# Kernel optimization log

Measured on AMD Instinct MI355X. Metric: run time of the kernel, lower is better.

## Reference

```python
import jax, jax.numpy as jnp
import numpy as np

B, S, D, H, HD = 4, 2048, 1024, 16, 64  # batch, seq, d_model, heads, head_dim


def setup_inputs() -> dict:
    key = jax.random.key(0)
    ks = jax.random.split(key, 9)
    scale = 0.02
    x = jax.random.normal(ks[0], (B, S, D), jnp.float32)
    Wq = jax.random.normal(ks[1], (D, H, HD), jnp.float32) * scale
    Wk = jax.random.normal(ks[2], (D, H, HD), jnp.float32) * scale
    Wv = jax.random.normal(ks[3], (D, H, HD), jnp.float32) * scale
    bq = jax.random.normal(ks[4], (H, HD), jnp.float32) * scale
    bk = jax.random.normal(ks[5], (H, HD), jnp.float32) * scale
    bv = jax.random.normal(ks[6], (H, HD), jnp.float32) * scale
    Wo = jax.random.normal(ks[7], (H, HD, D), jnp.float32) * scale
    bo = jax.random.normal(ks[8], (D,), jnp.float32) * scale
    return {"x": x, "Wq": Wq, "bq": bq, "Wk": Wk, "bk": bk,
            "Wv": Wv, "bv": bv, "Wo": Wo, "bo": bo}


def reference(x, Wq, bq, Wk, bk, Wv, bv, Wo, bo):
    # QKV projections -> (B, S, H, HD)
    q = jnp.einsum("bsd,dhe->bshe", x, Wq) + bq
    k = jnp.einsum("bsd,dhe->bshe", x, Wk) + bk
    v = jnp.einsum("bsd,dhe->bshe", x, Wv) + bv
    # scaled dot-product attention (deterministic, no mask/bias)
    q = q / jnp.sqrt(jnp.asarray(HD, q.dtype))
    scores = jnp.einsum("bqhd,bkhd->bhqk", q, k)  # (B, H, S, S)
    attn = jax.nn.softmax(scores, axis=-1)
    ctx = jnp.einsum("bhqk,bkhd->bqhd", attn, v)  # (B, S, H, HD)
    # output projection -> (B, S, D)
    return jnp.einsum("bqhd,hdo->bqo", ctx, Wo) + bo
```

## Files before the change

### kernel.cpp

```cpp
#include <hip/hip_runtime.h>


typedef unsigned short u16;
typedef __attribute__((ext_vector_type(4))) float f32x4;
typedef __attribute__((ext_vector_type(8))) short s16x8;
typedef __attribute__((ext_vector_type(4))) unsigned short u16x4;
typedef __attribute__((ext_vector_type(2))) unsigned int u32x2;
typedef __attribute__((ext_vector_type(4))) unsigned int u32x4;

#define DEV __device__ __forceinline__

#if __has_builtin(__builtin_amdgcn_exp2f)
#define EXP2(x) __builtin_amdgcn_exp2f(x)
#else
#define EXP2(x) exp2f(x)
#endif

DEV u16 f2b(float f) {
  unsigned u = __float_as_uint(f);
  u += 0x7fffu + ((u >> 16) & 1u);
  return (u16)(u >> 16);
}

DEV unsigned pack2(float a, float b) {
#if __has_builtin(__builtin_amdgcn_cvt_pk_bf16_f32)
  typedef __attribute__((ext_vector_type(2))) __bf16 bf16x2;
  bf16x2 r = __builtin_amdgcn_cvt_pk_bf16_f32(a, b);
  return __builtin_bit_cast(unsigned, r);
#else
  return (unsigned)f2b(a) | ((unsigned)f2b(b) << 16);
#endif
}

DEV void async16(const void* g, void* l) {
  __builtin_amdgcn_global_load_lds(
      (const __attribute__((address_space(1))) unsigned int*)g,
      (__attribute__((address_space(3))) unsigned int*)l, 16, 0, 0);
}

__global__ void k_cast(const float* __restrict__ x, u16* __restrict__ xb) {
  int i = (blockIdx.x * 256 + threadIdx.x) * 4;
  float4 v = *(const float4*)(x + i);
  u16x4 o;
  o.x = f2b(v.x); o.y = f2b(v.y); o.z = f2b(v.z); o.w = f2b(v.w);
  *(u16x4*)(xb + i) = o;
}

__global__ void k_packw_all(const float* __restrict__ Wq, const float* __restrict__ Wk,
                            const float* __restrict__ Wv, const float* __restrict__ Wo,
                            u16* __restrict__ wt, u16* __restrict__ wot, float qscale) {
  const float* src; u16* dst; float scale = 1.0f;
  switch (blockIdx.z) {
    case 0: src = Wq; dst = wt; scale = qscale; break;
    case 1: src = Wk; dst = wt + 1024 * 1024; break;
    case 2: src = Wv; dst = wt + 2 * 1024 * 1024; break;
    default: src = Wo; dst = wot; break;
  }
  __shared__ float tile[32][33];
  int t = threadIdx.x;
  int k0 = blockIdx.x * 32, n0 = blockIdx.y * 32;
  int c = t & 31, r0 = t >> 5;
#pragma unroll
  for (int p = 0; p < 4; ++p) {
    int r = p * 8 + r0;
    tile[r][c] = src[(size_t)(k0 + r) * 1024 + n0 + c] * scale;
  }
  __syncthreads();
#pragma unroll
  for (int p = 0; p < 4; ++p) {
    int r = p * 8 + r0;
    dst[(size_t)(n0 + r) * 1024 + k0 + c] = f2b(tile[c][r]);
  }
}

__global__ void k_packbias(const float* __restrict__ bq, const float* __restrict__ bk,
                           const float* __restrict__ bv, float* __restrict__ out,
                           float qscale) {
  int t = blockIdx.x * 256 + threadIdx.x;
  float v = (t < 1024) ? bq[t] * qscale : (t < 2048 ? bk[t - 1024] : bv[t - 2048]);
  out[t] = v;
}

template <int MODE>
__global__ __launch_bounds__(256, 2) void k_gemm_bt(
    const u16* __restrict__ A, const u16* __restrict__ Bt,
    const float* __restrict__ bias, void* __restrict__ Cout, u16* __restrict__ VT,
    int K, int ldC, int nbase) {
  __shared__ u16 SH[16384];
  u16* As = SH;
  u16* Bs = SH + 8192;
  const int t = threadIdx.x;
  const int w = t >> 6, l = t & 63;
  const int lane15 = l & 15, quad = l >> 4;
  const int m0 = blockIdx.x * 128, n0 = nbase + blockIdx.y * 128;
  const int wm = (w >> 1) * 64, wn = (w & 1) * 64;

  const int srow = t >> 3, cp = t & 7;
  const u16* aSrc[4]; const u16* bSrc[4]; int ldsOff[4];
#pragma unroll
  for (int i = 0; i < 4; ++i) {
    int row = i * 32 + srow;
    int gc = cp ^ (row & 7);
    aSrc[i] = A + (size_t)(m0 + row) * K + gc * 8;
    bSrc[i] = Bt + (size_t)(n0 + row) * K + gc * 8;
    ldsOff[i] = (i * 32 + w * 8) * 64;
  }

  f32x4 acc[4][4] = {};

  for (int kk = 0; kk < K; kk += 64) {
#pragma unroll
    for (int i = 0; i < 4; ++i) async16(aSrc[i] + kk, As + ldsOff[i]);
#pragma unroll
    for (int i = 0; i < 4; ++i) async16(bSrc[i] + kk, Bs + ldsOff[i]);
    __builtin_amdgcn_s_waitcnt(0);
    __syncthreads();

#pragma unroll
    for (int ks = 0; ks < 2; ++ks) {
      s16x8 af[4], bf[4];
#pragma unroll
      for (int mi = 0; mi < 4; ++mi) {
        int r = wm + mi * 16 + lane15;
        int c = ks * 4 + quad;
        af[mi] = *(const s16x8*)(As + r * 64 + (c ^ (r & 7)) * 8);
      }
#pragma unroll
      for (int ni = 0; ni < 4; ++ni) {
        int r = wn + ni * 16 + lane15;
        int c = ks * 4 + quad;
        bf[ni] = *(const s16x8*)(Bs + r * 64 + (c ^ (r & 7)) * 8);
      }
#pragma unroll
      for (int mi = 0; mi < 4; ++mi)
#pragma unroll
        for (int ni = 0; ni < 4; ++ni)
          acc[mi][ni] = (MODE == 0)
              ? __builtin_amdgcn_mfma_f32_16x16x32_bf16(bf[ni], af[mi], acc[mi][ni], 0, 0, 0)
              : __builtin_amdgcn_mfma_f32_16x16x32_bf16(af[mi], bf[ni], acc[mi][ni], 0, 0, 0);
    }
    __syncthreads();
  }

  if (MODE == 0) {
    u16* W = SH + w * 4096;
#pragma unroll
    for (int ni = 0; ni < 4; ++ni) {
      int gnb = n0 + wn + ni * 16 + quad * 4;
      float4 bb = *(const float4*)(bias + gnb);
#pragma unroll
      for (int mi = 0; mi < 4; ++mi) {
        int mloc = mi * 16 + lane15;
        int nloc = ni * 16 + quad * 4;
        int blk = (nloc >> 3) ^ (mloc & 7);
        u32x2 o;
        o.x = pack2(acc[mi][ni][0] + bb.x, acc[mi][ni][1] + bb.y);
        o.y = pack2(acc[mi][ni][2] + bb.z, acc[mi][ni][3] + bb.w);
        *(u32x2*)(W + mloc * 64 + blk * 8 + (quad & 1) * 4) = o;
      }
    }
    const int l8 = l & 7, lr = l >> 3;
#pragma unroll
    for (int it = 0; it < 8; ++it) {
      int mloc = it * 8 + lr;
      int lb = l8 ^ (mloc & 7);
      s16x8 v = *(const s16x8*)(W + mloc * 64 + l8 * 8);
      int gm = m0 + wm + mloc;
      *(s16x8*)((u16*)Cout + (size_t)gm * ldC + n0 + wn + lb * 8) = v;
    }
  } else if (MODE == 1) {
#pragma unroll
    for (int ni = 0; ni < 4; ++ni) {
      int gn = n0 + wn + ni * 16 + lane15;
      float bb = bias[gn];
#pragma unroll
      for (int mi = 0; mi < 4; ++mi) {
        int gmBase = m0 + wm + mi * 16 + quad * 4;
#pragma unroll
        for (int r = 0; r < 4; ++r)
          ((float*)Cout)[(size_t)(gmBase + r) * ldC + gn] = acc[mi][ni][r] + bb;
      }
    }
  } else {
    u16* W = SH + w * 4096;
#pragma unroll
    for (int ni = 0; ni < 4; ++ni) {
      int gn = n0 + wn + ni * 16 + lane15;
      float bb = bias[gn];
#pragma unroll
      for (int mi = 0; mi < 4; ++mi) {
        int nloc = ni * 16 + lane15;
        int mloc = mi * 16 + quad * 4;
        int blk = (mloc >> 3) ^ (nloc & 7);
        u32x2 o;
        o.x = pack2(acc[mi][ni][0] + bb, acc[mi][ni][1] + bb);
        o.y = pack2(acc[mi][ni][2] + bb, acc[mi][ni][3] + bb);
        *(u32x2*)(W + nloc * 64 + blk * 8 + (quad & 1) * 4) = o;
      }
    }
    const int l8 = l & 7, lr = l >> 3;
#pragma unroll
    for (int it = 0; it < 8; ++it) {
      int nloc = it * 8 + lr;
      int lb = l8 ^ (nloc & 7);
      s16x8 v = *(const s16x8*)(W + nloc * 64 + l8 * 8);
      int gv = (n0 - 2048) + wn + nloc;
      int hh = gv >> 6, hd = gv & 63;
      int gm = m0 + wm + lb * 8;
      int bb2 = gm >> 11, s = gm & 2047;
      *(s16x8*)(VT + (((size_t)(bb2 * 16 + hh) * 64 + hd) * 2048 + s)) = v;
    }
  }
}

__global__ __launch_bounds__(512, 4) void k_flash(
    const u16* __restrict__ qkv, const u16* __restrict__ vt, u16* __restrict__ ctx) {
  __shared__ u16 S[2][8192];
  const int t = threadIdx.x;
  const int w = t >> 6, l = t & 63;
  const int lane15 = l & 15, quad = l >> 4;
  const int bh = blockIdx.x, qt = blockIdx.y;
  const int b = bh >> 4, h = bh & 15;

  int qrow[2];
  s16x8 qf[2][2];
#pragma unroll
  for (int T = 0; T < 2; ++T) {
    qrow[T] = b * 2048 + qt * 256 + w * 32 + T * 16 + lane15;
    const u16* qp = qkv + (size_t)qrow[T] * 2048 + h * 64 + quad * 8;
    qf[T][0] = *(const s16x8*)(qp);
    qf[T][1] = *(const s16x8*)(qp + 32);
  }

  const int srow = t >> 3, cp = t & 7;
  const int xks = (srow & 3) | (((srow >> 3) & 1) << 2);
  const u16* kSrc = qkv + (size_t)(b * 2048 + srow) * 2048 + 1024 + h * 64 + (cp ^ xks) * 8;
  const u16* vSrc = vt + (size_t)bh * (64 * 2048) + (size_t)srow * 2048 + (cp ^ (srow & 7)) * 8;
  const int kOff = w * 512;
  const int vOff = 4096 + w * 512;

  const int kr = (lane15 >> 2) * 8 + (lane15 & 3);
  f32x4 O[2][4] = {};
  float lsum[2] = {0.0f, 0.0f};
  const f32x4 ZERO4 = {};

  async16(kSrc, &S[0][kOff]);
  async16(vSrc, &S[0][vOff]);

  for (int jt = 0; jt < 32; ++jt) {
    __builtin_amdgcn_s_waitcnt(0);
    __syncthreads();
    const u16* Sb = S[jt & 1];
    if (jt < 31) {
      const size_t kAdv = (size_t)(jt + 1) * 64 * 2048;
      const int vAdv = (jt + 1) * 64;
      u16* D = S[(jt & 1) ^ 1];
      async16(kSrc + kAdv, D + kOff);
      async16(vSrc + vAdv, D + vOff);
    }

    f32x4 st[2][4];
    __builtin_amdgcn_s_setprio(1);
#pragma unroll
    for (int tt = 0; tt < 4; ++tt) {
      int rr = kr + (tt & 1) * 4 + (tt >> 1) * 32;
      int xk = (rr & 3) | (((rr >> 3) & 1) << 2);
      s16x8 kf = *(const s16x8*)(Sb + rr * 64 + ((0 * 4 + quad) ^ xk) * 8);
#pragma unroll
      for (int T = 0; T < 2; ++T)
        st[T][tt] = __builtin_amdgcn_mfma_f32_16x16x32_bf16(kf, qf[T][0], ZERO4, 0, 0, 0);
    }
#pragma unroll
    for (int tt = 0; tt < 4; ++tt) {
      int rr = kr + (tt & 1) * 4 + (tt >> 1) * 32;
      int xk = (rr & 3) | (((rr >> 3) & 1) << 2);
      s16x8 kf = *(const s16x8*)(Sb + rr * 64 + ((1 * 4 + quad) ^ xk) * 8);
#pragma unroll
      for (int T = 0; T < 2; ++T)
        st[T][tt] = __builtin_amdgcn_mfma_f32_16x16x32_bf16(kf, qf[T][1], st[T][tt], 0, 0, 0);
    }
    __builtin_amdgcn_s_setprio(0);

#pragma unroll
    for (int ks = 0; ks < 2; ++ks) {
      s16x8 pf[2];
#pragma unroll
      for (int T = 0; T < 2; ++T) {
        float p0 = EXP2(st[T][2 * ks][0]), p1 = EXP2(st[T][2 * ks][1]);
        float p2 = EXP2(st[T][2 * ks][2]), p3 = EXP2(st[T][2 * ks][3]);
        float p4 = EXP2(st[T][2 * ks + 1][0]), p5 = EXP2(st[T][2 * ks + 1][1]);
        float p6 = EXP2(st[T][2 * ks + 1][2]), p7 = EXP2(st[T][2 * ks + 1][3]);
        lsum[T] += ((p0 + p1) + (p2 + p3)) + ((p4 + p5) + (p6 + p7));
        u32x4 pu = {pack2(p0, p1), pack2(p2, p3), pack2(p4, p5), pack2(p6, p7)};
        pf[T] = __builtin_bit_cast(s16x8, pu);
      }
      const u16* Vh = Sb + 4096;
      int c7 = ks * 4 + quad;
      __builtin_amdgcn_s_setprio(1);
#pragma unroll
      for (int co = 0; co < 4; ++co) {
        int rr = co * 16 + lane15;
        s16x8 vf = *(const s16x8*)(Vh + rr * 64 + ((c7 ^ (rr & 7))) * 8);
#pragma unroll
        for (int T = 0; T < 2; ++T)
          O[T][co] = __builtin_amdgcn_mfma_f32_16x16x32_bf16(vf, pf[T], O[T][co], 0, 0, 0);
      }
      __builtin_amdgcn_s_setprio(0);
    }
  }

#pragma unroll
  for (int T = 0; T < 2; ++T) {
    lsum[T] += __shfl_xor(lsum[T], 16);
    lsum[T] += __shfl_xor(lsum[T], 32);
  }

#pragma unroll
  for (int T = 0; T < 2; ++T) {
    float inv = 1.0f / lsum[T];
#pragma unroll
    for (int co = 0; co < 4; ++co) {
      u32x2 o;
      o.x = pack2(O[T][co][0] * inv, O[T][co][1] * inv);
      o.y = pack2(O[T][co][2] * inv, O[T][co][3] * inv);
      *(u32x2*)(ctx + (size_t)qrow[T] * 1024 + h * 64 + co * 16 + quad * 4) = o;
    }
  }
}

static constexpr size_t OFF_XB  = 0;
static constexpr size_t OFF_WT  = OFF_XB + (16u << 20);
static constexpr size_t OFF_WOT = OFF_WT + (6u << 20);
static constexpr size_t OFF_B3  = OFF_WOT + (2u << 20);
static constexpr size_t OFF_QKV = OFF_B3 + (1u << 20);
static constexpr size_t OFF_VT  = OFF_QKV + (32u << 20);
static constexpr size_t OFF_CTX = OFF_VT + (16u << 20);

extern "C" void kernel_launch(void* const* d_in, const int* in_sizes, int n_in,
                              void* d_out, int out_size, void* d_ws, size_t ws_size,
                              hipStream_t stream) {
  const float* x  = (const float*)d_in[0];
  const float* Wq = (const float*)d_in[1];
  const float* bq = (const float*)d_in[2];
  const float* Wk = (const float*)d_in[3];
  const float* bk = (const float*)d_in[4];
  const float* Wv = (const float*)d_in[5];
  const float* bv = (const float*)d_in[6];
  const float* Wo = (const float*)d_in[7];
  const float* bo = (const float*)d_in[8];
  char* ws = (char*)d_ws;
  u16* xb    = (u16*)(ws + OFF_XB);
  u16* wt    = (u16*)(ws + OFF_WT);
  u16* wot   = (u16*)(ws + OFF_WOT);
  float* b3  = (float*)(ws + OFF_B3);
  u16* qkv   = (u16*)(ws + OFF_QKV);
  u16* vtb   = (u16*)(ws + OFF_VT);
  u16* ctx   = (u16*)(ws + OFF_CTX);
  float* out = (float*)d_out;

  const float QSCALE = 0.125f * 1.44269504f;

  k_cast<<<8192, 256, 0, stream>>>(x, xb);
  k_packw_all<<<dim3(32, 32, 4), 256, 0, stream>>>(Wq, Wk, Wv, Wo, wt, wot, QSCALE);
  k_packbias<<<12, 256, 0, stream>>>(bq, bk, bv, b3, QSCALE);
  k_gemm_bt<0><<<dim3(64, 16), 256, 0, stream>>>(xb, wt, b3, qkv, nullptr, 1024, 2048, 0);
  k_gemm_bt<2><<<dim3(64, 8), 256, 0, stream>>>(xb, wt, b3, nullptr, vtb, 1024, 2048, 2048);
  k_flash<<<dim3(64, 8), 512, 0, stream>>>(qkv, vtb, ctx);
  k_gemm_bt<1><<<dim3(64, 8), 256, 0, stream>>>(ctx, wot, bo, out, nullptr, 1024, 1024, 0);
}
```

Measured before the change: 265.8 us.

## Load K/V fragments directly from global memory in flash kernel, drop LDS staging

Removes the double-buffered shared-memory staging of K and V tiles and the per-iteration barrier. Each wave now loads its MFMA operand fragments straight from global memory, relying on L1/L2 caching across waves. The block is halved to 256 threads over 128 query rows, with the grid doubled to match. This trades barrier and LDS overhead for redundant global loads by every wave and the latency of exposed global reads.

```diff
diff --git a/kernel.cpp b/kernel.cpp
--- a/kernel.cpp
+++ b/kernel.cpp
@@ -213,9 +213,8 @@
   }
 }
 
-__global__ __launch_bounds__(512, 4) void k_flash(
+__global__ __launch_bounds__(256, 4) void k_flash(
     const u16* __restrict__ qkv, const u16* __restrict__ vt, u16* __restrict__ ctx) {
-  __shared__ u16 S[2][8192];
   const int t = threadIdx.x;
   const int w = t >> 6, l = t & 63;
   const int lane15 = l & 15, quad = l >> 4;
@@ -226,63 +225,58 @@
   s16x8 qf[2][2];
 #pragma unroll
   for (int T = 0; T < 2; ++T) {
-    qrow[T] = b * 2048 + qt * 256 + w * 32 + T * 16 + lane15;
+    qrow[T] = b * 2048 + qt * 128 + w * 32 + T * 16 + lane15;
     const u16* qp = qkv + (size_t)qrow[T] * 2048 + h * 64 + quad * 8;
     qf[T][0] = *(const s16x8*)(qp);
     qf[T][1] = *(const s16x8*)(qp + 32);
   }
 
-  const int srow = t >> 3, cp = t & 7;
-  const int xks = (srow & 3) | (((srow >> 3) & 1) << 2);
-  const u16* kSrc = qkv + (size_t)(b * 2048 + srow) * 2048 + 1024 + h * 64 + (cp ^ xks) * 8;
-  const u16* vSrc = vt + (size_t)bh * (64 * 2048) + (size_t)srow * 2048 + (cp ^ (srow & 7)) * 8;
-  const int kOff = w * 512;
-  const int vOff = 4096 + w * 512;
-
   const int kr = (lane15 >> 2) * 8 + (lane15 & 3);
+  const u16* kBase = qkv + (size_t)b * 2048 * 2048 + 1024 + h * 64 + quad * 8;
+  const u16* vBase = vt + (size_t)bh * (64 * 2048) + quad * 8;
+  int kOffE[4], vOffE[4];
+#pragma unroll
+  for (int tt = 0; tt < 4; ++tt) kOffE[tt] = (kr + (tt & 1) * 4 + (tt >> 1) * 32) * 2048;
+#pragma unroll
+  for (int co = 0; co < 4; ++co) vOffE[co] = (co * 16 + lane15) * 2048;
+
   f32x4 O[2][4] = {};
   float lsum[2] = {0.0f, 0.0f};
   const f32x4 ZERO4 = {};
 
-  async16(kSrc, &S[0][kOff]);
-  async16(vSrc, &S[0][vOff]);
-
   for (int jt = 0; jt < 32; ++jt) {
-    __builtin_amdgcn_s_waitcnt(0);
-    __syncthreads();
-    const u16* Sb = S[jt & 1];
-    if (jt < 31) {
-      const size_t kAdv = (size_t)(jt + 1) * 64 * 2048;
-      const int vAdv = (jt + 1) * 64;
-      u16* D = S[(jt & 1) ^ 1];
-      async16(kSrc + kAdv, D + kOff);
-      async16(vSrc + vAdv, D + vOff);
+    const u16* kT = kBase + (size_t)jt * 64 * 2048;
+    const u16* vT = vBase + jt * 64;
+
+    s16x8 kf0[4], kf1[4];
+#pragma unroll
+    for (int tt = 0; tt < 4; ++tt) {
+      const u16* p = kT + kOffE[tt];
+      kf0[tt] = *(const s16x8*)(p);
+      kf1[tt] = *(const s16x8*)(p + 32);
     }
 
     f32x4 st[2][4];
     __builtin_amdgcn_s_setprio(1);
 #pragma unroll
-    for (int tt = 0; tt < 4; ++tt) {
-      int rr = kr + (tt & 1) * 4 + (tt >> 1) * 32;
-      int xk = (rr & 3) | (((rr >> 3) & 1) << 2);
-      s16x8 kf = *(const s16x8*)(Sb + rr * 64 + ((0 * 4 + quad) ^ xk) * 8);
+    for (int tt = 0; tt < 4; ++tt)
 #pragma unroll
       for (int T = 0; T < 2; ++T)
-        st[T][tt] = __builtin_amdgcn_mfma_f32_16x16x32_bf16(kf, qf[T][0], ZERO4, 0, 0, 0);
-    }
-#pragma unroll
-    for (int tt = 0; tt < 4; ++tt) {
-      int rr = kr + (tt & 1) * 4 + (tt >> 1) * 32;
-      int xk = (rr & 3) | (((rr >> 3) & 1) << 2);
-      s16x8 kf = *(const s16x8*)(Sb + rr * 64 + ((1 * 4 + quad) ^ xk) * 8);
+        st[T][tt] = __builtin_amdgcn_mfma_f32_16x16x32_bf16(kf0[tt], qf[T][0], ZERO4, 0, 0, 0);
+#pragma unroll
+    for (int tt = 0; tt < 4; ++tt)
 #pragma unroll
       for (int T = 0; T < 2; ++T)
-        st[T][tt] = __builtin_amdgcn_mfma_f32_16x16x32_bf16(kf, qf[T][1], st[T][tt], 0, 0, 0);
-    }
+        st[T][tt] = __builtin_amdgcn_mfma_f32_16x16x32_bf16(kf1[tt], qf[T][1], st[T][tt], 0, 0, 0);
     __builtin_amdgcn_s_setprio(0);
 
 #pragma unroll
     for (int ks = 0; ks < 2; ++ks) {
+      s16x8 vf[4];
+#pragma unroll
+      for (int co = 0; co < 4; ++co)
+        vf[co] = *(const s16x8*)(vT + vOffE[co] + ks * 32);
+
       s16x8 pf[2];
 #pragma unroll
       for (int T = 0; T < 2; ++T) {
@@ -294,17 +288,13 @@
         u32x4 pu = {pack2(p0, p1), pack2(p2, p3), pack2(p4, p5), pack2(p6, p7)};
         pf[T] = __builtin_bit_cast(s16x8, pu);
       }
-      const u16* Vh = Sb + 4096;
-      int c7 = ks * 4 + quad;
+
       __builtin_amdgcn_s_setprio(1);
 #pragma unroll
-      for (int co = 0; co < 4; ++co) {
-        int rr = co * 16 + lane15;
-        s16x8 vf = *(const s16x8*)(Vh + rr * 64 + ((c7 ^ (rr & 7))) * 8);
+      for (int co = 0; co < 4; ++co)
 #pragma unroll
         for (int T = 0; T < 2; ++T)
-          O[T][co] = __builtin_amdgcn_mfma_f32_16x16x32_bf16(vf, pf[T], O[T][co], 0, 0, 0);
-      }
+          O[T][co] = __builtin_amdgcn_mfma_f32_16x16x32_bf16(vf[co], pf[T], O[T][co], 0, 0, 0);
       __builtin_amdgcn_s_setprio(0);
     }
   }
@@ -365,6 +355,6 @@
   k_packbias<<<12, 256, 0, stream>>>(bq, bk, bv, b3, QSCALE);
   k_gemm_bt<0><<<dim3(64, 16), 256, 0, stream>>>(xb, wt, b3, qkv, nullptr, 1024, 2048, 0);
   k_gemm_bt<2><<<dim3(64, 8), 256, 0, stream>>>(xb, wt, b3, nullptr, vtb, 1024, 2048, 2048);
-  k_flash<<<dim3(64, 8), 512, 0, stream>>>(qkv, vtb, ctx);
+  k_flash<<<dim3(64, 16), 256, 0, stream>>>(qkv, vtb, ctx);
   k_gemm_bt<1><<<dim3(64, 8), 256, 0, stream>>>(ctx, wot, bo, out, nullptr, 1024, 1024, 0);
 }
```

Result: slower. 504.9 us (+90.0%).

## Fuse QKV projections into one double-buffered 128x256 GEMM kernel

Applied to the files above, without the earlier changes.

Replaces the two QKV projection GEMM launches (Q/K to a row-major buffer, V to a transposed buffer) with a single kernel. It uses 512 threads, 128x256 tiles and double-buffered LDS, so the next K-tile loads asynchronously while the current one runs MFMA. MFMA sections run at raised wave priority and use split barriers. This removes one launch and the exposed load latency of the old single-buffered loop, at the cost of 96KB LDS and one block per CU.

```diff
diff --git a/kernel.cpp b/kernel.cpp
--- a/kernel.cpp
+++ b/kernel.cpp
@@ -79,6 +79,144 @@
   int t = blockIdx.x * 256 + threadIdx.x;
   float v = (t < 1024) ? bq[t] * qscale : (t < 2048 ? bk[t - 1024] : bv[t - 2048]);
   out[t] = v;
+}
+
+#define QKV_STAGE(DST, kn)                                                \
+  { const int ko = (kn) * 64;                                             \
+    async16(aB + ko,          (DST) + 0 * 4096 + w * 512);                \
+    async16(aB + 65536 + ko,  (DST) + 4096 + w * 512);                    \
+    async16(bB + ko,          (DST) + 8192 + w * 512);                    \
+    async16(bB + 65536 + ko,  (DST) + 12288 + w * 512);                   \
+    async16(bB + 131072 + ko, (DST) + 16384 + w * 512);                   \
+    async16(bB + 196608 + ko, (DST) + 20480 + w * 512); }
+
+#define QKV_LOADFRAG(SRC, ks)                                             \
+  { _Pragma("unroll") for (int mi = 0; mi < 4; ++mi) {                    \
+      int r = wmE + mi * 16 + lane15;                                     \
+      int c = (ks) * 4 + quad;                                            \
+      af[mi] = *(const s16x8*)((SRC) + r * 64 + (c ^ (r & 7)) * 8);       \
+    }                                                                     \
+    _Pragma("unroll") for (int ni = 0; ni < 4; ++ni) {                    \
+      int rn = wnE + ni * 16 + lane15;                                    \
+      int c = (ks) * 4 + quad;                                            \
+      bf[ni] = *(const s16x8*)((SRC) + 8192 + rn * 64 + (c ^ (rn & 7)) * 8); \
+    } }
+
+#define QKV_MFMA()                                                        \
+  { __builtin_amdgcn_s_setprio(1);                                        \
+    if (swapped) {                                                        \
+      _Pragma("unroll") for (int mi = 0; mi < 4; ++mi)                    \
+        _Pragma("unroll") for (int ni = 0; ni < 4; ++ni)                  \
+          acc[mi][ni] = __builtin_amdgcn_mfma_f32_16x16x32_bf16(          \
+              bf[ni], af[mi], acc[mi][ni], 0, 0, 0);                      \
+    } else {                                                              \
+      _Pragma("unroll") for (int mi = 0; mi < 4; ++mi)                    \
+        _Pragma("unroll") for (int ni = 0; ni < 4; ++ni)                  \
+          acc[mi][ni] = __builtin_amdgcn_mfma_f32_16x16x32_bf16(          \
+              af[mi], bf[ni], acc[mi][ni], 0, 0, 0);                      \
+    }                                                                     \
+    __builtin_amdgcn_s_setprio(0); }
+
+#define QKV_TILE(SRC, DST, kt, DO_STAGE)                                  \
+  { if (DO_STAGE) QKV_STAGE(DST, (kt) + 1);                               \
+    s16x8 af[4], bf[4];                                                   \
+    QKV_LOADFRAG(SRC, 0);                                                 \
+    __builtin_amdgcn_s_barrier();                                         \
+    QKV_MFMA();                                                           \
+    __builtin_amdgcn_s_barrier();                                         \
+    QKV_LOADFRAG(SRC, 1);                                                 \
+    __builtin_amdgcn_s_barrier();                                         \
+    QKV_MFMA();                                                           \
+    if (DO_STAGE) asm volatile("s_waitcnt vmcnt(0)" ::: "memory");        \
+    __builtin_amdgcn_s_barrier(); }
+
+__global__ __launch_bounds__(512, 1) void k_gemm_qkv(
+    const u16* __restrict__ A, const u16* __restrict__ Bt,
+    const float* __restrict__ bias, u16* __restrict__ qkv,
+    u16* __restrict__ VT) {
+  __shared__ u16 S0[24576];
+  __shared__ u16 S1[24576];
+  const int t = threadIdx.x;
+  const int w = t >> 6, l = t & 63;
+  const int lane15 = l & 15, quad = l >> 4;
+  const int m0 = blockIdx.x * 128, n0 = blockIdx.y * 256;
+  const bool swapped = (n0 < 2048);
+  const int wmE = (w >> 2) * 64, wnE = (w & 3) * 64;
+
+  const int srow8 = w * 8 + (l >> 3);
+  const int gc = (l & 7) ^ ((l >> 3) & 7);
+  const u16* aB = A + (size_t)(m0 + srow8) * 1024 + gc * 8;
+  const u16* bB = Bt + (size_t)(n0 + srow8) * 1024 + gc * 8;
+
+  f32x4 acc[4][4] = {};
+
+  QKV_STAGE(S0, 0);
+  asm volatile("s_waitcnt vmcnt(0)" ::: "memory");
+  __builtin_amdgcn_s_barrier();
+
+#pragma unroll 1
+  for (int kp = 0; kp < 7; ++kp) {
+    QKV_TILE(S0, S1, 2 * kp, true);
+    QKV_TILE(S1, S0, 2 * kp + 1, true);
+  }
+  QKV_TILE(S0, S1, 14, true);
+  QKV_TILE(S1, S0, 15, false);
+
+  u16* W = (w < 6) ? (S0 + w * 4096) : (S1 + (w - 6) * 4096);
+  const int l8 = l & 7, lr = l >> 3;
+
+  if (swapped) {
+#pragma unroll
+    for (int ni = 0; ni < 4; ++ni) {
+      int gnb = n0 + wnE + ni * 16 + quad * 4;
+      float4 bb = *(const float4*)(bias + gnb);
+#pragma unroll
+      for (int mi = 0; mi < 4; ++mi) {
+        int mloc = mi * 16 + lane15;
+        int nloc = ni * 16 + quad * 4;
+        int blk = (nloc >> 3) ^ (mloc & 7);
+        u32x2 o;
+        o.x = pack2(acc[mi][ni][0] + bb.x, acc[mi][ni][1] + bb.y);
+        o.y = pack2(acc[mi][ni][2] + bb.z, acc[mi][ni][3] + bb.w);
+        *(u32x2*)(W + mloc * 64 + blk * 8 + (quad & 1) * 4) = o;
+      }
+    }
+#pragma unroll
+    for (int it = 0; it < 8; ++it) {
+      int mloc = it * 8 + lr;
+      int lb = l8 ^ (mloc & 7);
+      s16x8 v = *(const s16x8*)(W + mloc * 64 + l8 * 8);
+      int gm = m0 + wmE + mloc;
+      *(s16x8*)(qkv + (size_t)gm * 2048 + n0 + wnE + lb * 8) = v;
+    }
+  } else {
+#pragma unroll
+    for (int ni = 0; ni < 4; ++ni) {
+      int gn = n0 + wnE + ni * 16 + lane15;
+      float bb = bias[gn];
+#pragma unroll
+      for (int mi = 0; mi < 4; ++mi) {
+        int nloc = ni * 16 + lane15;
+        int mloc = mi * 16 + quad * 4;
+        int blk = (mloc >> 3) ^ (nloc & 7);
+        u32x2 o;
+        o.x = pack2(acc[mi][ni][0] + bb, acc[mi][ni][1] + bb);
+        o.y = pack2(acc[mi][ni][2] + bb, acc[mi][ni][3] + bb);
+        *(u32x2*)(W + nloc * 64 + blk * 8 + (quad & 1) * 4) = o;
+      }
+    }
+#pragma unroll
+    for (int it = 0; it < 8; ++it) {
+      int nloc = it * 8 + lr;
+      int lb = l8 ^ (nloc & 7);
+      s16x8 v = *(const s16x8*)(W + nloc * 64 + l8 * 8);
+      int gv = (n0 - 2048) + wnE + nloc;
+      int hh = gv >> 6, hd = gv & 63;
+      int gm = m0 + wmE + lb * 8;
+      int bb2 = gm >> 11, s = gm & 2047;
+      *(s16x8*)(VT + (((size_t)(bb2 * 16 + hh) * 64 + hd) * 2048 + s)) = v;
+    }
+  }
 }
 
 template <int MODE>
@@ -100,9 +238,9 @@
 #pragma unroll
   for (int i = 0; i < 4; ++i) {
     int row = i * 32 + srow;
-    int gc = cp ^ (row & 7);
-    aSrc[i] = A + (size_t)(m0 + row) * K + gc * 8;
-    bSrc[i] = Bt + (size_t)(n0 + row) * K + gc * 8;
+    int gcs = cp ^ (row & 7);
+    aSrc[i] = A + (size_t)(m0 + row) * K + gcs * 8;
+    bSrc[i] = Bt + (size_t)(n0 + row) * K + gcs * 8;
     ldsOff[i] = (i * 32 + w * 8) * 64;
   }
 
@@ -142,33 +280,7 @@
     __syncthreads();
   }
 
-  if (MODE == 0) {
-    u16* W = SH + w * 4096;
-#pragma unroll
-    for (int ni = 0; ni < 4; ++ni) {
-      int gnb = n0 + wn + ni * 16 + quad * 4;
-      float4 bb = *(const float4*)(bias + gnb);
-#pragma unroll
-      for (int mi = 0; mi < 4; ++mi) {
-        int mloc = mi * 16 + lane15;
-        int nloc = ni * 16 + quad * 4;
-        int blk = (nloc >> 3) ^ (mloc & 7);
-        u32x2 o;
-        o.x = pack2(acc[mi][ni][0] + bb.x, acc[mi][ni][1] + bb.y);
-        o.y = pack2(acc[mi][ni][2] + bb.z, acc[mi][ni][3] + bb.w);
-        *(u32x2*)(W + mloc * 64 + blk * 8 + (quad & 1) * 4) = o;
-      }
-    }
-    const int l8 = l & 7, lr = l >> 3;
-#pragma unroll
-    for (int it = 0; it < 8; ++it) {
-      int mloc = it * 8 + lr;
-      int lb = l8 ^ (mloc & 7);
-      s16x8 v = *(const s16x8*)(W + mloc * 64 + l8 * 8);
-      int gm = m0 + wm + mloc;
-      *(s16x8*)((u16*)Cout + (size_t)gm * ldC + n0 + wn + lb * 8) = v;
-    }
-  } else if (MODE == 1) {
+  if (MODE == 1) {
 #pragma unroll
     for (int ni = 0; ni < 4; ++ni) {
       int gn = n0 + wn + ni * 16 + lane15;
@@ -180,35 +292,6 @@
         for (int r = 0; r < 4; ++r)
           ((float*)Cout)[(size_t)(gmBase + r) * ldC + gn] = acc[mi][ni][r] + bb;
       }
-    }
-  } else {
-    u16* W = SH + w * 4096;
-#pragma unroll
-    for (int ni = 0; ni < 4; ++ni) {
-      int gn = n0 + wn + ni * 16 + lane15;
-      float bb = bias[gn];
-#pragma unroll
-      for (int mi = 0; mi < 4; ++mi) {
-        int nloc = ni * 16 + lane15;
-        int mloc = mi * 16 + quad * 4;
-        int blk = (mloc >> 3) ^ (nloc & 7);
-        u32x2 o;
-        o.x = pack2(acc[mi][ni][0] + bb, acc[mi][ni][1] + bb);
-        o.y = pack2(acc[mi][ni][2] + bb, acc[mi][ni][3] + bb);
-        *(u32x2*)(W + nloc * 64 + blk * 8 + (quad & 1) * 4) = o;
-      }
-    }
-    const int l8 = l & 7, lr = l >> 3;
-#pragma unroll
-    for (int it = 0; it < 8; ++it) {
-      int nloc = it * 8 + lr;
-      int lb = l8 ^ (nloc & 7);
-      s16x8 v = *(const s16x8*)(W + nloc * 64 + l8 * 8);
-      int gv = (n0 - 2048) + wn + nloc;
-      int hh = gv >> 6, hd = gv & 63;
-      int gm = m0 + wm + lb * 8;
-      int bb2 = gm >> 11, s = gm & 2047;
-      *(s16x8*)(VT + (((size_t)(bb2 * 16 + hh) * 64 + hd) * 2048 + s)) = v;
     }
   }
 }
@@ -363,8 +446,7 @@
   k_cast<<<8192, 256, 0, stream>>>(x, xb);
   k_packw_all<<<dim3(32, 32, 4), 256, 0, stream>>>(Wq, Wk, Wv, Wo, wt, wot, QSCALE);
   k_packbias<<<12, 256, 0, stream>>>(bq, bk, bv, b3, QSCALE);
-  k_gemm_bt<0><<<dim3(64, 16), 256, 0, stream>>>(xb, wt, b3, qkv, nullptr, 1024, 2048, 0);
-  k_gemm_bt<2><<<dim3(64, 8), 256, 0, stream>>>(xb, wt, b3, nullptr, vtb, 1024, 2048, 2048);
+  k_gemm_qkv<<<dim3(64, 12), 512, 0, stream>>>(xb, wt, b3, qkv, vtb);
   k_flash<<<dim3(64, 8), 512, 0, stream>>>(qkv, vtb, ctx);
   k_gemm_bt<1><<<dim3(64, 8), 256, 0, stream>>>(ctx, wot, bo, out, nullptr, 1024, 1024, 0);
 }
```

After: 279.6 us. 5.2% more time.

## Fuse QKV projection GEMMs into one triple-buffered 128x256 tile kernel

Applied to the files above, without the earlier changes.

Replaces the two QKV projection GEMM launches (QK and V-transposed) with a single kernel. It uses 512 threads, 128x256 output tiles and a three-stage async global-to-LDS pipeline with partial vmcnt waits and raised MFMA priority. The goal is to overlap loads with MFMA work, cut one launch and a tail, and get more reuse per tile. The cost is a much larger LDS footprint (about 144 KB), which limits the kernel to one block per CU, plus a branch per tile on output layout.

```diff
diff --git a/kernel.cpp b/kernel.cpp
--- a/kernel.cpp
+++ b/kernel.cpp
@@ -79,6 +79,148 @@
   int t = blockIdx.x * 256 + threadIdx.x;
   float v = (t < 1024) ? bq[t] * qscale : (t < 2048 ? bk[t - 1024] : bv[t - 2048]);
   out[t] = v;
+}
+
+#define QSTAGE(BUFB, ktv)                                               \
+  { const int ko = (ktv) * 64;                                          \
+    async16(aP + ko,          S + (BUFB) + ldsW);                       \
+    async16(aP + ko + 65536,  S + (BUFB) + 4096 + ldsW);                \
+    async16(bP + ko,          S + (BUFB) + 8192 + ldsW);                \
+    async16(bP + ko + 65536,  S + (BUFB) + 12288 + ldsW);               \
+    async16(bP + ko + 131072, S + (BUFB) + 16384 + ldsW);               \
+    async16(bP + ko + 196608, S + (BUFB) + 20480 + ldsW); }
+
+#define QCOMP(BUFB)                                                     \
+  { _Pragma("unroll")                                                   \
+    for (int ks = 0; ks < 2; ++ks) {                                    \
+      s16x8 af[4], bf[4];                                               \
+      _Pragma("unroll") for (int mi = 0; mi < 4; ++mi) {                \
+        int r = wmE + mi * 16 + lane15;                                 \
+        int c = ks * 4 + quad;                                          \
+        af[mi] = *(const s16x8*)(S + (BUFB) + r * 64 + (c ^ (r & 7)) * 8); \
+      }                                                                 \
+      _Pragma("unroll") for (int ni = 0; ni < 4; ++ni) {                \
+        int rn = wnE + ni * 16 + lane15;                                \
+        int c = ks * 4 + quad;                                          \
+        bf[ni] = *(const s16x8*)(S + (BUFB) + 8192 + rn * 64 + (c ^ (rn & 7)) * 8); \
+      }                                                                 \
+      __builtin_amdgcn_s_setprio(1);                                    \
+      if (swapped) {                                                    \
+        _Pragma("unroll") for (int mi = 0; mi < 4; ++mi)                \
+          _Pragma("unroll") for (int ni = 0; ni < 4; ++ni)              \
+            acc[mi][ni] = __builtin_amdgcn_mfma_f32_16x16x32_bf16(      \
+                bf[ni], af[mi], acc[mi][ni], 0, 0, 0);                  \
+      } else {                                                          \
+        _Pragma("unroll") for (int mi = 0; mi < 4; ++mi)                \
+          _Pragma("unroll") for (int ni = 0; ni < 4; ++ni)              \
+            acc[mi][ni] = __builtin_amdgcn_mfma_f32_16x16x32_bf16(      \
+                af[mi], bf[ni], acc[mi][ni], 0, 0, 0);                  \
+      }                                                                 \
+      __builtin_amdgcn_s_setprio(0);                                    \
+    } }
+
+#define GTILE(CURB, NXTB, ktv, DOSTAGE)                                 \
+  { __builtin_amdgcn_s_barrier();                                       \
+    if (DOSTAGE) {                                                      \
+      QSTAGE(NXTB, (ktv) + 2);                                          \
+      asm volatile("s_waitcnt vmcnt(6)" ::: "memory");                  \
+    } else {                                                            \
+      asm volatile("s_waitcnt vmcnt(0)" ::: "memory");                  \
+    }                                                                   \
+    QCOMP(CURB) }
+
+__global__ __launch_bounds__(512, 1) void k_gemm_qkv(
+    const u16* __restrict__ A, const u16* __restrict__ Bt,
+    const float* __restrict__ bias, u16* __restrict__ qkv,
+    u16* __restrict__ VT) {
+  __shared__ u16 S[73728];
+  const int t = threadIdx.x;
+  const int w = t >> 6, l = t & 63;
+  const int lane15 = l & 15, quad = l >> 4;
+  const int m0 = blockIdx.x * 128, n0 = blockIdx.y * 256;
+  const bool swapped = (n0 < 2048);
+  const int wmE = (w >> 2) * 64, wnE = (w & 3) * 64;
+
+  const int gc = (l & 7) ^ ((l >> 3) & 7);
+  const u16* aP = A  + (size_t)(m0 + w * 8 + (l >> 3)) * 1024 + gc * 8;
+  const u16* bP = Bt + (size_t)(n0 + w * 8 + (l >> 3)) * 1024 + gc * 8;
+  const int ldsW = w * 512;
+
+  f32x4 acc[4][4] = {};
+
+  QSTAGE(0, 0);
+  QSTAGE(24576, 1);
+  asm volatile("s_waitcnt vmcnt(6)" ::: "memory");
+
+#pragma unroll 1
+  for (int j = 0; j < 4; ++j) {
+    int kt = 3 * j;
+    GTILE(0,     49152, kt,     1);
+    GTILE(24576, 0,     kt + 1, 1);
+    GTILE(49152, 24576, kt + 2, 1);
+  }
+  GTILE(0,     49152, 12, 1);
+  GTILE(24576, 0,     13, 1);
+  GTILE(49152, 24576, 14, 0);
+  GTILE(0,     0,     15, 0);
+
+  __syncthreads();
+
+  u16* W = S + w * 4096;
+  const int l8 = l & 7, lr = l >> 3;
+
+  if (swapped) {
+#pragma unroll
+    for (int ni = 0; ni < 4; ++ni) {
+      int gnb = n0 + wnE + ni * 16 + quad * 4;
+      float4 bb = *(const float4*)(bias + gnb);
+#pragma unroll
+      for (int mi = 0; mi < 4; ++mi) {
+        int mloc = mi * 16 + lane15;
+        int nloc = ni * 16 + quad * 4;
+        int blk = (nloc >> 3) ^ (mloc & 7);
+        u32x2 o;
+        o.x = pack2(acc[mi][ni][0] + bb.x, acc[mi][ni][1] + bb.y);
+        o.y = pack2(acc[mi][ni][2] + bb.z, acc[mi][ni][3] + bb.w);
+        *(u32x2*)(W + mloc * 64 + blk * 8 + (quad & 1) * 4) = o;
+      }
+    }
+#pragma unroll
+    for (int it = 0; it < 8; ++it) {
+      int mloc = it * 8 + lr;
+      int lb = l8 ^ (mloc & 7);
+      s16x8 v = *(const s16x8*)(W + mloc * 64 + l8 * 8);
+      int gm = m0 + wmE + mloc;
+      *(s16x8*)(qkv + (size_t)gm * 2048 + n0 + wnE + lb * 8) = v;
+    }
+  } else {
+#pragma unroll
+    for (int ni = 0; ni < 4; ++ni) {
+      int gn = n0 + wnE + ni * 16 + lane15;
+      float bb = bias[gn];
+#pragma unroll
+      for (int mi = 0; mi < 4; ++mi) {
+        int nloc = ni * 16 + lane15;
+        int mloc = mi * 16 + quad * 4;
+        int blk = (mloc >> 3) ^ (nloc & 7);
+        u32x2 o;
+        o.x = pack2(acc[mi][ni][0] + bb, acc[mi][ni][1] + bb);
+        o.y = pack2(acc[mi][ni][2] + bb, acc[mi][ni][3] + bb);
+        *(u32x2*)(W + nloc * 64 + blk * 8 + (quad & 1) * 4) = o;
+      }
+    }
+#pragma unroll
+    for (int it = 0; it < 8; ++it) {
+      int nloc = it * 8 + lr;
+      int lb = l8 ^ (nloc & 7);
+      s16x8 v = *(const s16x8*)(W + nloc * 64 + l8 * 8);
+      int gv = (n0 - 2048) + wnE + nloc;
+      int hh = gv >> 6, hd = gv & 63;
+      int gm = m0 + wmE + lb * 8;
+      int bb2 = gm >> 11, s = gm & 2047;
+      *(s16x8*)(VT + (((size_t)(bb2 * 16 + hh) * 64 + hd) * 2048 + s)) = v;
+    }
+  }
 }
 
 template <int MODE>
@@ -100,9 +242,9 @@
 #pragma unroll
   for (int i = 0; i < 4; ++i) {
     int row = i * 32 + srow;
-    int gc = cp ^ (row & 7);
-    aSrc[i] = A + (size_t)(m0 + row) * K + gc * 8;
-    bSrc[i] = Bt + (size_t)(n0 + row) * K + gc * 8;
+    int gcs = cp ^ (row & 7);
+    aSrc[i] = A + (size_t)(m0 + row) * K + gcs * 8;
+    bSrc[i] = Bt + (size_t)(n0 + row) * K + gcs * 8;
     ldsOff[i] = (i * 32 + w * 8) * 64;
   }
 
@@ -142,33 +284,7 @@
     __syncthreads();
   }
 
-  if (MODE == 0) {
-    u16* W = SH + w * 4096;
-#pragma unroll
-    for (int ni = 0; ni < 4; ++ni) {
-      int gnb = n0 + wn + ni * 16 + quad * 4;
-      float4 bb = *(const float4*)(bias + gnb);
-#pragma unroll
-      for (int mi = 0; mi < 4; ++mi) {
-        int mloc = mi * 16 + lane15;
-        int nloc = ni * 16 + quad * 4;
-        int blk = (nloc >> 3) ^ (mloc & 7);
-        u32x2 o;
-        o.x = pack2(acc[mi][ni][0] + bb.x, acc[mi][ni][1] + bb.y);
-        o.y = pack2(acc[mi][ni][2] + bb.z, acc[mi][ni][3] + bb.w);
-        *(u32x2*)(W + mloc * 64 + blk * 8 + (quad & 1) * 4) = o;
-      }
-    }
-    const int l8 = l & 7, lr = l >> 3;
-#pragma unroll
-    for (int it = 0; it < 8; ++it) {
-      int mloc = it * 8 + lr;
-      int lb = l8 ^ (mloc & 7);
-      s16x8 v = *(const s16x8*)(W + mloc * 64 + l8 * 8);
-      int gm = m0 + wm + mloc;
-      *(s16x8*)((u16*)Cout + (size_t)gm * ldC + n0 + wn + lb * 8) = v;
-    }
-  } else if (MODE == 1) {
+  if (MODE == 1) {
 #pragma unroll
     for (int ni = 0; ni < 4; ++ni) {
       int gn = n0 + wn + ni * 16 + lane15;
@@ -180,35 +296,6 @@
         for (int r = 0; r < 4; ++r)
           ((float*)Cout)[(size_t)(gmBase + r) * ldC + gn] = acc[mi][ni][r] + bb;
       }
-    }
-  } else {
-    u16* W = SH + w * 4096;
-#pragma unroll
-    for (int ni = 0; ni < 4; ++ni) {
-      int gn = n0 + wn + ni * 16 + lane15;
-      float bb = bias[gn];
-#pragma unroll
-      for (int mi = 0; mi < 4; ++mi) {
-        int nloc = ni * 16 + lane15;
-        int mloc = mi * 16 + quad * 4;
-        int blk = (mloc >> 3) ^ (nloc & 7);
-        u32x2 o;
-        o.x = pack2(acc[mi][ni][0] + bb, acc[mi][ni][1] + bb);
-        o.y = pack2(acc[mi][ni][2] + bb, acc[mi][ni][3] + bb);
-        *(u32x2*)(W + nloc * 64 + blk * 8 + (quad & 1) * 4) = o;
-      }
-    }
-    const int l8 = l & 7, lr = l >> 3;
-#pragma unroll
-    for (int it = 0; it < 8; ++it) {
-      int nloc = it * 8 + lr;
-      int lb = l8 ^ (nloc & 7);
-      s16x8 v = *(const s16x8*)(W + nloc * 64 + l8 * 8);
-      int gv = (n0 - 2048) + wn + nloc;
-      int hh = gv >> 6, hd = gv & 63;
-      int gm = m0 + wm + lb * 8;
-      int bb2 = gm >> 11, s = gm & 2047;
-      *(s16x8*)(VT + (((size_t)(bb2 * 16 + hh) * 64 + hd) * 2048 + s)) = v;
     }
   }
 }
@@ -363,8 +450,7 @@
   k_cast<<<8192, 256, 0, stream>>>(x, xb);
   k_packw_all<<<dim3(32, 32, 4), 256, 0, stream>>>(Wq, Wk, Wv, Wo, wt, wot, QSCALE);
   k_packbias<<<12, 256, 0, stream>>>(bq, bk, bv, b3, QSCALE);
-  k_gemm_bt<0><<<dim3(64, 16), 256, 0, stream>>>(xb, wt, b3, qkv, nullptr, 1024, 2048, 0);
-  k_gemm_bt<2><<<dim3(64, 8), 256, 0, stream>>>(xb, wt, b3, nullptr, vtb, 1024, 2048, 2048);
+  k_gemm_qkv<<<dim3(64, 12), 512, 0, stream>>>(xb, wt, b3, qkv, vtb);
   k_flash<<<dim3(64, 8), 512, 0, stream>>>(qkv, vtb, ctx);
   k_gemm_bt<1><<<dim3(64, 8), 256, 0, stream>>>(ctx, wot, bo, out, nullptr, 1024, 1024, 0);
 }
```

Result: no change. 264.7 us (-0.4%).
